# Kernel tuning notes

Hardware: AMD Instinct MI355X
Metric: run time of the kernel (lower is better)

## Reference

```python
import jax, jax.numpy as jnp
import numpy as np


def setup_inputs() -> dict:
    key = jax.random.key(0)
    k1, k2, k3, k4 = jax.random.split(key, 4)
    B, L, D_IN, D_OUT, E = 512, 50, 768, 300, 8
    x = jax.random.normal(k1, (B, L, D_IN), dtype=jnp.float32)
    w_gate = jax.random.normal(k2, (D_IN, E), dtype=jnp.float32) * 0.02
    expert_w = jax.random.normal(k3, (E, D_OUT, D_IN), dtype=jnp.float32) * 0.02
    expert_bias = jax.random.normal(k4, (E, L, D_IN), dtype=jnp.float32) * 0.02
    return {"x": x, "w_gate": w_gate, "expert_w": expert_w, "expert_bias": expert_bias}


def reference(x, w_gate, expert_w, expert_bias):
    # Gating (eval mode: noisy gating disabled) -> softmax over experts
    gates = jax.nn.softmax(x @ w_gate, axis=-1)  # [B, L, E]
    # DTRLayer: lin(x - bias) = x @ W^T - bias @ W^T (linearity avoids [B,L,E,D_in] intermediate)
    xw = jnp.einsum('bli,eoi->bleo', x, expert_w)           # [B, L, E, O]
    bw = jnp.einsum('eli,eoi->leo', expert_bias, expert_w)  # [L, E, O]
    expert_out = xw - bw[None]                              # [B, L, E, O]
    # Gate-weighted sum over experts
    return jnp.einsum('ble,bleo->blo', gates, expert_out)   # [B, L, O]
```

## Files before the change

kernel.cpp:

```cpp
#include <hip/hip_runtime.h>
#include <hip/hip_bf16.h>

#define BATCH   512
#define LSEQ    50
#define DIN     768
#define DOUT    300
#define NEXP    8
#define NTOK    (BATCH * LSEQ)

typedef __bf16 bf16_t;
typedef __attribute__((ext_vector_type(8))) __bf16 bf16x8;
typedef __attribute__((ext_vector_type(4))) float f32x4;

#define GLDS16(g, l) __builtin_amdgcn_global_load_lds( \
    (__attribute__((address_space(1))) void*)(g), \
    (__attribute__((address_space(3))) void*)(l), 16, 0, 0)

static __device__ __forceinline__ unsigned short f2bf(float f) {
    unsigned u = __float_as_uint(f);
    u = (u + 0x7fff + ((u >> 16) & 1)) >> 16;
    return (unsigned short)u;
}

#define PREP_GATE_BLOCKS (NTOK / 4)
#define PREP_BW_BLOCKS   ((2 * NEXP * DOUT) / 4)

__global__ __launch_bounds__(256) void prep_kernel(
    const float* __restrict__ x, const float* __restrict__ wg,
    const float* __restrict__ bias, const float* __restrict__ W,
    unsigned short* __restrict__ xb, float* __restrict__ gates,
    float* __restrict__ bw, unsigned short* __restrict__ wb)
{
    const int tid  = threadIdx.x;
    const int lane = tid & 63;

    if (blockIdx.x < PREP_GATE_BLOCKS) {
        __shared__ float wgT[NEXP][DIN + 4];
        #pragma unroll
        for (int r = 0; r < 6; ++r) {
            int j = tid + 256 * r;
            float4 v = ((const float4*)wg)[j];
            int i  = j >> 1;
            int e0 = (j & 1) * 4;
            wgT[e0 + 0][i] = v.x;
            wgT[e0 + 1][i] = v.y;
            wgT[e0 + 2][i] = v.z;
            wgT[e0 + 3][i] = v.w;
        }
        __syncthreads();

        int t = blockIdx.x * 4 + (tid >> 6);
        const float4* xr = (const float4*)(x + (size_t)t * DIN);
        ushort4* xo = (ushort4*)(xb + (size_t)t * DIN);

        float acc[NEXP];
        #pragma unroll
        for (int e = 0; e < NEXP; e++) acc[e] = 0.0f;

        #pragma unroll
        for (int k = 0; k < 3; ++k) {
            int i4 = lane + 64 * k;
            float4 v = xr[i4];
            ushort4 u;
            u.x = f2bf(v.x); u.y = f2bf(v.y); u.z = f2bf(v.z); u.w = f2bf(v.w);
            xo[i4] = u;
            #pragma unroll
            for (int e = 0; e < NEXP; ++e) {
                float4 wv = *(const float4*)&wgT[e][4 * i4];
                acc[e] += v.x * wv.x + v.y * wv.y + v.z * wv.z + v.w * wv.w;
            }
        }
        #pragma unroll
        for (int e = 0; e < NEXP; e++) {
            #pragma unroll
            for (int m = 32; m > 0; m >>= 1) acc[e] += __shfl_xor(acc[e], m, 64);
        }
        float mx = acc[0];
        #pragma unroll
        for (int e = 1; e < NEXP; e++) mx = fmaxf(mx, acc[e]);
        float ex[NEXP]; float s = 0.0f;
        #pragma unroll
        for (int e = 0; e < NEXP; e++) { ex[e] = __expf(acc[e] - mx); s += ex[e]; }
        float inv = 1.0f / s;
        if (lane == 0) {
            #pragma unroll
            for (int e = 0; e < NEXP; e++) gates[(size_t)t * NEXP + e] = ex[e] * inv;
        }
    } else {
        int wid  = (blockIdx.x - PREP_GATE_BLOCKS) * 4 + (tid >> 6);
        int half = wid & 1;
        int eo   = wid >> 1;
        int e = eo / DOUT, o = eo % DOUT;

        const float4* wr = (const float4*)(W + ((size_t)e * DOUT + o) * DIN);
        float4 w4[3];
        #pragma unroll
        for (int k = 0; k < 3; ++k) w4[k] = wr[lane + 64 * k];

        if (half == 0) {
            ushort4* wo = (ushort4*)(wb + ((size_t)e * DOUT + o) * DIN);
            #pragma unroll
            for (int k = 0; k < 3; ++k) {
                ushort4 u;
                u.x = f2bf(w4[k].x); u.y = f2bf(w4[k].y);
                u.z = f2bf(w4[k].z); u.w = f2bf(w4[k].w);
                wo[lane + 64 * k] = u;
            }
        }

        int l0 = 25 * half;
        for (int l = l0; l < l0 + 25; ++l) {
            const float4* br = (const float4*)(bias + ((size_t)e * LSEQ + l) * DIN);
            float acc = 0.0f;
            #pragma unroll
            for (int k = 0; k < 3; ++k) {
                float4 b = br[lane + 64 * k];
                acc += b.x * w4[k].x + b.y * w4[k].y + b.z * w4[k].z + b.w * w4[k].w;
            }
            #pragma unroll
            for (int m = 32; m > 0; m >>= 1) acc += __shfl_xor(acc, m, 64);
            if (lane == 0) bw[((size_t)l * NEXP + e) * DOUT + o] = acc;
        }
    }
}

#define GTM 256
#define GTO 16
#define GBK 32
#define GKIT (DIN / GBK)
#define NRT  (NTOK / GTM)
#define NOT  19
#define RPG  13
#define NSLOT (8 * RPG * NOT)

#define BUFB 24576

__global__ __launch_bounds__(256, 2) void moe_mfma_kernel(
    const bf16_t* __restrict__ xb, const bf16_t* __restrict__ wb,
    const float* __restrict__ gates, const float* __restrict__ bw,
    float* __restrict__ out)
{
    const int bid  = blockIdx.x;
    const int g    = bid & 7;
    const int slot = bid >> 3;
    const int r_in = slot / NOT;
    const int o_t  = slot - NOT * r_in;
    const int r_t  = g * RPG + r_in;
    if (r_t >= NRT) return;
    const int o0 = o_t * GTO;
    const int t0 = r_t * GTM;

    __shared__ __align__(16) char lds[2 * BUFB];

    const int tid  = threadIdx.x;
    const int w    = tid >> 6;
    const int lane = tid & 63;

    const int srow4 = lane >> 2;
    const int c16   = 16 * ((lane & 3) ^ ((lane >> 4) & 3));

    const char* xg[4];
    #pragma unroll
    for (int j = 0; j < 4; ++j)
        xg[j] = (const char*)xb + (size_t)(t0 + 64 * w + 16 * j + srow4) * (DIN * 2) + c16;

    const char* wq[2];
    #pragma unroll
    for (int j = 0; j < 2; ++j) {
        int n = 32 * w + 16 * j + srow4;
        int e = n >> 4;
        int o = o0 + (n & 15); if (o >= DOUT) o = DOUT - 1;
        wq[j] = (const char*)wb + (size_t)(e * DOUT + o) * (DIN * 2) + c16;
    }

    const int m = lane & 15, q = lane >> 4;
    const int sw = 16 * (q ^ ((m >> 2) & 3));
    int aoff[4], boff[8];
    #pragma unroll
    for (int rf = 0; rf < 4; ++rf) aoff[rf] = 64 * (64 * w + 16 * rf + m) + sw;
    #pragma unroll
    for (int cf = 0; cf < 8; ++cf) boff[cf] = 16384 + 64 * (16 * cf + m) + sw;

    f32x4 acc[4][8] = {};

    {
        char* xl = lds + 4096 * w;
        char* wl = lds + 16384 + 2048 * w;
        #pragma unroll
        for (int j = 0; j < 4; ++j) { GLDS16(xg[j], xl + 1024 * j); xg[j] += 64; }
        #pragma unroll
        for (int j = 0; j < 2; ++j) { GLDS16(wq[j], wl + 1024 * j); wq[j] += 64; }
    }

    for (int it = 0; it < GKIT; ++it) {
        const int cur = it & 1;
        if (it + 1 < GKIT) {
            char* nb = lds + BUFB * (cur ^ 1);
            char* xl = nb + 4096 * w;
            char* wl = nb + 16384 + 2048 * w;
            #pragma unroll
            for (int j = 0; j < 4; ++j) { GLDS16(xg[j], xl + 1024 * j); xg[j] += 64; }
            #pragma unroll
            for (int j = 0; j < 2; ++j) { GLDS16(wq[j], wl + 1024 * j); wq[j] += 64; }
            asm volatile("s_waitcnt vmcnt(6)" ::: "memory");
        } else {
            asm volatile("s_waitcnt vmcnt(0)" ::: "memory");
        }
        __builtin_amdgcn_s_barrier();
        __builtin_amdgcn_sched_barrier(0);

        const char* cb = lds + BUFB * cur;
        bf16x8 a[4];
        #pragma unroll
        for (int rf = 0; rf < 4; ++rf) a[rf] = *(const bf16x8*)(cb + aoff[rf]);
        #pragma unroll
        for (int cf = 0; cf < 8; ++cf) {
            bf16x8 b = *(const bf16x8*)(cb + boff[cf]);
            #pragma unroll
            for (int rf = 0; rf < 4; ++rf)
                acc[rf][cf] = __builtin_amdgcn_mfma_f32_16x16x32_bf16(a[rf], b, acc[rf][cf], 0, 0, 0);
        }

        __builtin_amdgcn_sched_barrier(0);
        asm volatile("s_waitcnt lgkmcnt(0)" ::: "memory");
        __builtin_amdgcn_sched_barrier(0);
        __builtin_amdgcn_s_barrier();
    }

    const int o = o0 + m;
    if (o < DOUT) {
        #pragma unroll
        for (int rf = 0; rf < 4; ++rf) {
            #pragma unroll
            for (int r = 0; r < 4; ++r) {
                int t = t0 + 64 * w + 16 * rf + 4 * q + r;
                int l = t % LSEQ;
                float4 g0 = *(const float4*)(gates + (size_t)t * NEXP);
                float4 g1 = *(const float4*)(gates + (size_t)t * NEXP + 4);
                const float* bp = bw + (size_t)l * NEXP * DOUT + o;
                float s = 0.0f;
                s += g0.x * (acc[rf][0][r] - bp[0 * DOUT]);
                s += g0.y * (acc[rf][1][r] - bp[1 * DOUT]);
                s += g0.z * (acc[rf][2][r] - bp[2 * DOUT]);
                s += g0.w * (acc[rf][3][r] - bp[3 * DOUT]);
                s += g1.x * (acc[rf][4][r] - bp[4 * DOUT]);
                s += g1.y * (acc[rf][5][r] - bp[5 * DOUT]);
                s += g1.z * (acc[rf][6][r] - bp[6 * DOUT]);
                s += g1.w * (acc[rf][7][r] - bp[7 * DOUT]);
                out[(size_t)t * DOUT + o] = s;
            }
        }
    }
}

__global__ __launch_bounds__(256) void gates_kernel(
    const float* __restrict__ x, const float* __restrict__ wg,
    float* __restrict__ gates)
{
    int t    = blockIdx.x * 4 + (threadIdx.x >> 6);
    int lane = threadIdx.x & 63;
    const float* xr = x + (size_t)t * DIN;
    float acc[NEXP];
    #pragma unroll
    for (int e = 0; e < NEXP; e++) acc[e] = 0.0f;
    for (int i = lane; i < DIN; i += 64) {
        float xv = xr[i];
        const float* wr = wg + (size_t)i * NEXP;
        #pragma unroll
        for (int e = 0; e < NEXP; e++) acc[e] += xv * wr[e];
    }
    #pragma unroll
    for (int e = 0; e < NEXP; e++) {
        #pragma unroll
        for (int m = 32; m > 0; m >>= 1) acc[e] += __shfl_xor(acc[e], m, 64);
    }
    float mx = acc[0];
    #pragma unroll
    for (int e = 1; e < NEXP; e++) mx = fmaxf(mx, acc[e]);
    float ex[NEXP]; float s = 0.0f;
    #pragma unroll
    for (int e = 0; e < NEXP; e++) { ex[e] = __expf(acc[e] - mx); s += ex[e]; }
    float inv = 1.0f / s;
    if (lane == 0) {
        #pragma unroll
        for (int e = 0; e < NEXP; e++) gates[(size_t)t * NEXP + e] = ex[e] * inv;
    }
}

__global__ __launch_bounds__(256) void bw_kernel(
    const float* __restrict__ bias, const float* __restrict__ W,
    float* __restrict__ bw)
{
    int wave = blockIdx.x * 4 + (threadIdx.x >> 6);
    int lane = threadIdx.x & 63;
    int l   = wave / (NEXP * DOUT);
    int rem = wave % (NEXP * DOUT);
    int e   = rem / DOUT;
    int o   = rem % DOUT;
    const float4* br = (const float4*)(bias + ((size_t)e * LSEQ + l) * DIN);
    const float4* wr = (const float4*)(W    + ((size_t)e * DOUT + o) * DIN);
    float acc = 0.0f;
    #pragma unroll
    for (int k = 0; k < 3; ++k) {
        int i4 = lane + 64 * k;
        float4 b = br[i4], w = wr[i4];
        acc += b.x * w.x + b.y * w.y + b.z * w.z + b.w * w.w;
    }
    #pragma unroll
    for (int m = 32; m > 0; m >>= 1) acc += __shfl_xor(acc, m, 64);
    if (lane == 0) bw[((size_t)l * NEXP + e) * DOUT + o] = acc;
}

#define TM  64
#define TO  16
#define KT  32
#define KTP 36

__global__ __launch_bounds__(256) void moe_main_kernel(
    const float* __restrict__ x, const float* __restrict__ W,
    const float* __restrict__ gates, const float* __restrict__ bw,
    float* __restrict__ out)
{
    __shared__ float Xs[TM][KTP];
    __shared__ float Wls[128][KTP];
    const int tid = threadIdx.x;
    const int t0 = blockIdx.x * TM;
    const int o0 = blockIdx.y * TO;
    const int cg = tid & 15;
    const int tg = tid >> 4;
    const int lrow = tid >> 3;
    const int lk4  = (tid & 7) * 4;
    float acc[4][NEXP];
    #pragma unroll
    for (int i = 0; i < 4; i++)
        #pragma unroll
        for (int j = 0; j < NEXP; j++) acc[i][j] = 0.0f;
    for (int k0 = 0; k0 < DIN; k0 += KT) {
        #pragma unroll
        for (int r = 0; r < 2; r++) {
            int row = lrow + 32 * r;
            float4 v = *(const float4*)&x[((size_t)(t0 + row)) * DIN + k0 + lk4];
            *(float4*)&Xs[row][lk4] = v;
        }
        #pragma unroll
        for (int r = 0; r < 4; r++) {
            int nl = lrow + 32 * r;
            int e  = nl >> 4;
            int o  = o0 + (nl & 15);
            float4 v;
            if (o < DOUT)
                v = *(const float4*)&W[((size_t)e * DOUT + o) * DIN + k0 + lk4];
            else
                v = make_float4(0.f, 0.f, 0.f, 0.f);
            *(float4*)&Wls[nl][lk4] = v;
        }
        __syncthreads();
        #pragma unroll
        for (int k4 = 0; k4 < KT; k4 += 4) {
            float4 xa[4], wb4[NEXP];
            #pragma unroll
            for (int i = 0; i < 4; i++)
                xa[i] = *(const float4*)&Xs[tg + 16 * i][k4];
            #pragma unroll
            for (int j = 0; j < NEXP; j++)
                wb4[j] = *(const float4*)&Wls[cg + 16 * j][k4];
            #pragma unroll
            for (int i = 0; i < 4; i++)
                #pragma unroll
                for (int j = 0; j < NEXP; j++) {
                    acc[i][j] += xa[i].x * wb4[j].x;
                    acc[i][j] += xa[i].y * wb4[j].y;
                    acc[i][j] += xa[i].z * wb4[j].z;
                    acc[i][j] += xa[i].w * wb4[j].w;
                }
        }
        __syncthreads();
    }
    const int o = o0 + cg;
    if (o < DOUT) {
        #pragma unroll
        for (int i = 0; i < 4; i++) {
            int t = t0 + tg + 16 * i;
            int l = t % LSEQ;
            float s = 0.0f;
            #pragma unroll
            for (int j = 0; j < NEXP; j++) {
                float g = gates[(size_t)t * NEXP + j];
                s += g * (acc[i][j] - bw[((size_t)l * NEXP + j) * DOUT + o]);
            }
            out[(size_t)t * DOUT + o] = s;
        }
    }
}

extern "C" void kernel_launch(void* const* d_in, const int* in_sizes, int n_in,
                              void* d_out, int out_size, void* d_ws, size_t ws_size,
                              hipStream_t stream) {
    const float* x     = (const float*)d_in[0];
    const float* wgate = (const float*)d_in[1];
    const float* ew    = (const float*)d_in[2];
    const float* ebias = (const float*)d_in[3];
    float* out = (float*)d_out;

    const size_t n_gates = (size_t)NTOK * NEXP;
    const size_t n_bw    = (size_t)LSEQ * NEXP * DOUT;
    const size_t n_x     = (size_t)NTOK * DIN;
    const size_t n_w     = (size_t)NEXP * DOUT * DIN;

    float* gates = (float*)d_ws;
    float* bw    = gates + n_gates;
    bf16_t* xb   = (bf16_t*)(bw + n_bw);
    bf16_t* wbuf = xb + n_x;

    const size_t need = (n_gates + n_bw) * 4 + (n_x + n_w) * 2;

    if (ws_size >= need) {
        prep_kernel<<<PREP_GATE_BLOCKS + PREP_BW_BLOCKS, 256, 0, stream>>>(
            x, wgate, ebias, ew, (unsigned short*)xb, gates, bw, (unsigned short*)wbuf);
        moe_mfma_kernel<<<NSLOT, 256, 0, stream>>>(xb, wbuf, gates, bw, out);
    } else {
        gates_kernel<<<NTOK / 4, 256, 0, stream>>>(x, wgate, gates);
        bw_kernel<<<(LSEQ * NEXP * DOUT) / 4, 256, 0, stream>>>(ebias, ew, bw);
        dim3 grid(NTOK / TM, (DOUT + TO - 1) / TO);
        moe_main_kernel<<<grid, 256, 0, stream>>>(x, ew, gates, bw, out);
    }
}
```

Measured before the change: 262.2 us.

## Load X operand fragments directly from global into registers, stage only weights in LDS

Each wave now reads its own A-operand rows of x straight from global memory into registers in MFMA fragment layout, instead of staging them through LDS via global_load_lds. Only the expert weight tile stays double-buffered in LDS, which shrinks shared memory from 48KB to 16KB and removes the trailing barrier per iteration. The aim is to cut LDS traffic and barrier overhead and allow higher occupancy. The cost is that x loads become less coalesced (16-byte chunks per lane across rows) and their global latency is exposed within each iteration rather than prefetched one step ahead.

```diff
diff --git a/kernel.cpp b/kernel.cpp
--- a/kernel.cpp
+++ b/kernel.cpp
@@ -126,14 +126,12 @@
 
 #define GTM 256
 #define GTO 16
-#define GBK 32
-#define GKIT (DIN / GBK)
+#define GKIT (DIN / 32)
 #define NRT  (NTOK / GTM)
 #define NOT  19
 #define RPG  13
 #define NSLOT (8 * RPG * NOT)
-
-#define BUFB 24576
+#define BBUF 8192
 
 __global__ __launch_bounds__(256, 2) void moe_mfma_kernel(
     const bf16_t* __restrict__ xb, const bf16_t* __restrict__ wb,
@@ -150,7 +148,7 @@
     const int o0 = o_t * GTO;
     const int t0 = r_t * GTM;
 
-    __shared__ __align__(16) char lds[2 * BUFB];
+    __shared__ __align__(16) char lds[2 * BBUF];
 
     const int tid  = threadIdx.x;
     const int w    = tid >> 6;
@@ -158,11 +156,6 @@
 
     const int srow4 = lane >> 2;
     const int c16   = 16 * ((lane & 3) ^ ((lane >> 4) & 3));
-
-    const char* xg[4];
-    #pragma unroll
-    for (int j = 0; j < 4; ++j)
-        xg[j] = (const char*)xb + (size_t)(t0 + 64 * w + 16 * j + srow4) * (DIN * 2) + c16;
 
     const char* wq[2];
     #pragma unroll
@@ -175,56 +168,93 @@
 
     const int m = lane & 15, q = lane >> 4;
     const int sw = 16 * (q ^ ((m >> 2) & 3));
-    int aoff[4], boff[8];
-    #pragma unroll
-    for (int rf = 0; rf < 4; ++rf) aoff[rf] = 64 * (64 * w + 16 * rf + m) + sw;
-    #pragma unroll
-    for (int cf = 0; cf < 8; ++cf) boff[cf] = 16384 + 64 * (16 * cf + m) + sw;
+    int boff[8];
+    #pragma unroll
+    for (int cf = 0; cf < 8; ++cf) boff[cf] = (16 * cf + m) * 64 + sw;
+
+    const char* xga[4];
+    #pragma unroll
+    for (int rf = 0; rf < 4; ++rf)
+        xga[rf] = (const char*)xb + (size_t)(t0 + 64 * w + 16 * rf + m) * (DIN * 2) + q * 16;
 
     f32x4 acc[4][8] = {};
 
-    {
-        char* xl = lds + 4096 * w;
-        char* wl = lds + 16384 + 2048 * w;
-        #pragma unroll
-        for (int j = 0; j < 4; ++j) { GLDS16(xg[j], xl + 1024 * j); xg[j] += 64; }
-        #pragma unroll
-        for (int j = 0; j < 2; ++j) { GLDS16(wq[j], wl + 1024 * j); wq[j] += 64; }
-    }
+    GLDS16(wq[0], lds + 2048 * w);
+    GLDS16(wq[1], lds + 2048 * w + 1024);
+    #pragma unroll
+    for (int j = 0; j < 2; ++j) wq[j] += 64;
 
     for (int it = 0; it < GKIT; ++it) {
         const int cur = it & 1;
-        if (it + 1 < GKIT) {
-            char* nb = lds + BUFB * (cur ^ 1);
-            char* xl = nb + 4096 * w;
-            char* wl = nb + 16384 + 2048 * w;
-            #pragma unroll
-            for (int j = 0; j < 4; ++j) { GLDS16(xg[j], xl + 1024 * j); xg[j] += 64; }
-            #pragma unroll
-            for (int j = 0; j < 2; ++j) { GLDS16(wq[j], wl + 1024 * j); wq[j] += 64; }
-            asm volatile("s_waitcnt vmcnt(6)" ::: "memory");
-        } else {
-            asm volatile("s_waitcnt vmcnt(0)" ::: "memory");
-        }
+
+        bf16x8 a0 = *(const bf16x8*)(xga[0]);
+        bf16x8 a1 = *(const bf16x8*)(xga[1]);
+        bf16x8 a2 = *(const bf16x8*)(xga[2]);
+        bf16x8 a3 = *(const bf16x8*)(xga[3]);
+        #pragma unroll
+        for (int rf = 0; rf < 4; ++rf) xga[rf] += 64;
+
+        asm volatile("s_waitcnt vmcnt(4)" ::: "memory");
         __builtin_amdgcn_s_barrier();
         __builtin_amdgcn_sched_barrier(0);
 
-        const char* cb = lds + BUFB * cur;
-        bf16x8 a[4];
-        #pragma unroll
-        for (int rf = 0; rf < 4; ++rf) a[rf] = *(const bf16x8*)(cb + aoff[rf]);
-        #pragma unroll
-        for (int cf = 0; cf < 8; ++cf) {
-            bf16x8 b = *(const bf16x8*)(cb + boff[cf]);
-            #pragma unroll
-            for (int rf = 0; rf < 4; ++rf)
-                acc[rf][cf] = __builtin_amdgcn_mfma_f32_16x16x32_bf16(a[rf], b, acc[rf][cf], 0, 0, 0);
-        }
-
+        if (it + 1 < GKIT) {
+            char* nb = lds + BBUF * (cur ^ 1);
+            GLDS16(wq[0], nb + 2048 * w);
+            GLDS16(wq[1], nb + 2048 * w + 1024);
+            #pragma unroll
+            for (int j = 0; j < 2; ++j) wq[j] += 64;
+        }
+
+        const char* cb = lds + BBUF * cur;
+        bf16x8 b0 = *(const bf16x8*)(cb + boff[0]);
+        bf16x8 b1 = *(const bf16x8*)(cb + boff[1]);
+        bf16x8 b2 = *(const bf16x8*)(cb + boff[2]);
+        bf16x8 b3 = *(const bf16x8*)(cb + boff[3]);
+        bf16x8 b4 = *(const bf16x8*)(cb + boff[4]);
+        bf16x8 b5 = *(const bf16x8*)(cb + boff[5]);
+        bf16x8 b6 = *(const bf16x8*)(cb + boff[6]);
+        bf16x8 b7 = *(const bf16x8*)(cb + boff[7]);
+
+        if (it + 1 < GKIT) {
+            asm volatile("s_waitcnt vmcnt(2) lgkmcnt(0)" ::: "memory");
+        } else {
+            asm volatile("s_waitcnt vmcnt(0) lgkmcnt(0)" ::: "memory");
+        }
         __builtin_amdgcn_sched_barrier(0);
-        asm volatile("s_waitcnt lgkmcnt(0)" ::: "memory");
-        __builtin_amdgcn_sched_barrier(0);
-        __builtin_amdgcn_s_barrier();
+
+        acc[0][0] = __builtin_amdgcn_mfma_f32_16x16x32_bf16(a0, b0, acc[0][0], 0, 0, 0);
+        acc[0][1] = __builtin_amdgcn_mfma_f32_16x16x32_bf16(a0, b1, acc[0][1], 0, 0, 0);
+        acc[0][2] = __builtin_amdgcn_mfma_f32_16x16x32_bf16(a0, b2, acc[0][2], 0, 0, 0);
+        acc[0][3] = __builtin_amdgcn_mfma_f32_16x16x32_bf16(a0, b3, acc[0][3], 0, 0, 0);
+        acc[0][4] = __builtin_amdgcn_mfma_f32_16x16x32_bf16(a0, b4, acc[0][4], 0, 0, 0);
+        acc[0][5] = __builtin_amdgcn_mfma_f32_16x16x32_bf16(a0, b5, acc[0][5], 0, 0, 0);
+        acc[0][6] = __builtin_amdgcn_mfma_f32_16x16x32_bf16(a0, b6, acc[0][6], 0, 0, 0);
+        acc[0][7] = __builtin_amdgcn_mfma_f32_16x16x32_bf16(a0, b7, acc[0][7], 0, 0, 0);
+        acc[1][0] = __builtin_amdgcn_mfma_f32_16x16x32_bf16(a1, b0, acc[1][0], 0, 0, 0);
+        acc[1][1] = __builtin_amdgcn_mfma_f32_16x16x32_bf16(a1, b1, acc[1][1], 0, 0, 0);
+        acc[1][2] = __builtin_amdgcn_mfma_f32_16x16x32_bf16(a1, b2, acc[1][2], 0, 0, 0);
+        acc[1][3] = __builtin_amdgcn_mfma_f32_16x16x32_bf16(a1, b3, acc[1][3], 0, 0, 0);
+        acc[1][4] = __builtin_amdgcn_mfma_f32_16x16x32_bf16(a1, b4, acc[1][4], 0, 0, 0);
+        acc[1][5] = __builtin_amdgcn_mfma_f32_16x16x32_bf16(a1, b5, acc[1][5], 0, 0, 0);
+        acc[1][6] = __builtin_amdgcn_mfma_f32_16x16x32_bf16(a1, b6, acc[1][6], 0, 0, 0);
+        acc[1][7] = __builtin_amdgcn_mfma_f32_16x16x32_bf16(a1, b7, acc[1][7], 0, 0, 0);
+        acc[2][0] = __builtin_amdgcn_mfma_f32_16x16x32_bf16(a2, b0, acc[2][0], 0, 0, 0);
+        acc[2][1] = __builtin_amdgcn_mfma_f32_16x16x32_bf16(a2, b1, acc[2][1], 0, 0, 0);
+        acc[2][2] = __builtin_amdgcn_mfma_f32_16x16x32_bf16(a2, b2, acc[2][2], 0, 0, 0);
+        acc[2][3] = __builtin_amdgcn_mfma_f32_16x16x32_bf16(a2, b3, acc[2][3], 0, 0, 0);
+        acc[2][4] = __builtin_amdgcn_mfma_f32_16x16x32_bf16(a2, b4, acc[2][4], 0, 0, 0);
+        acc[2][5] = __builtin_amdgcn_mfma_f32_16x16x32_bf16(a2, b5, acc[2][5], 0, 0, 0);
+        acc[2][6] = __builtin_amdgcn_mfma_f32_16x16x32_bf16(a2, b6, acc[2][6], 0, 0, 0);
+        acc[2][7] = __builtin_amdgcn_mfma_f32_16x16x32_bf16(a2, b7, acc[2][7], 0, 0, 0);
+        acc[3][0] = __builtin_amdgcn_mfma_f32_16x16x32_bf16(a3, b0, acc[3][0], 0, 0, 0);
+        acc[3][1] = __builtin_amdgcn_mfma_f32_16x16x32_bf16(a3, b1, acc[3][1], 0, 0, 0);
+        acc[3][2] = __builtin_amdgcn_mfma_f32_16x16x32_bf16(a3, b2, acc[3][2], 0, 0, 0);
+        acc[3][3] = __builtin_amdgcn_mfma_f32_16x16x32_bf16(a3, b3, acc[3][3], 0, 0, 0);
+        acc[3][4] = __builtin_amdgcn_mfma_f32_16x16x32_bf16(a3, b4, acc[3][4], 0, 0, 0);
+        acc[3][5] = __builtin_amdgcn_mfma_f32_16x16x32_bf16(a3, b5, acc[3][5], 0, 0, 0);
+        acc[3][6] = __builtin_amdgcn_mfma_f32_16x16x32_bf16(a3, b6, acc[3][6], 0, 0, 0);
+        acc[3][7] = __builtin_amdgcn_mfma_f32_16x16x32_bf16(a3, b7, acc[3][7], 0, 0, 0);
     }
 
     const int o = o0 + m;
```

Result: slower. 277.0 us (+5.7%).
